# Kernel tuning notes

Measured on AMD Instinct MI355X. Metric: run time of the kernel, lower is better.

Reference implementation:

```python
import jax, jax.numpy as jnp
import numpy as np

EMB = 64
NUM_LAYERS = 2


def _mlp_embed(x, shift, scale, w1, b1, w2, b2):
    # PreNormLayer: (x + shift) * scale, then Linear-ReLU-Linear-ReLU
    x = (x + shift) * scale
    x = jax.nn.relu(x @ w1 + b1)
    return jax.nn.relu(x @ w2 + b2)


def _sage_conv(x_src, x_dst, src_idx, dst_idx, ll_w, ll_b, lr_w):
    # PyG SAGEConv: mean-aggregate gathered source features at destinations,
    # out = lin_l(mean) + lin_r(x_dst); lin_l has bias, lin_r does not.
    n_dst = x_dst.shape[0]
    msgs = x_src[src_idx]                                   # [E, D] gather
    ssum = jax.ops.segment_sum(msgs, dst_idx, num_segments=n_dst)
    cnt = jax.ops.segment_sum(jnp.ones(src_idx.shape[0], x_src.dtype),
                              dst_idx, num_segments=n_dst)
    mean = ssum / jnp.maximum(cnt, 1.0)[:, None]            # [n_dst, D]
    return mean @ ll_w + ll_b + x_dst @ lr_w


def setup_inputs() -> dict:
    key = jax.random.key(0)
    ks = jax.random.split(key, 20)
    n_cons, n_var, n_edges = 100_000, 200_000, 2_000_000
    cons_nf, var_nf, edge_nf = 5, 19, 1

    def lin(k, fan_in, fan_out):
        return jax.random.normal(k, (fan_in, fan_out), jnp.float32) / np.sqrt(fan_in)

    inp = {
        'cons_x': jax.random.normal(ks[0], (n_cons, cons_nf), jnp.float32),
        'var_x': jax.random.normal(ks[1], (n_var, var_nf), jnp.float32),
        'edge_attr': jax.random.normal(ks[2], (n_edges, edge_nf), jnp.float32),
        'edge_index': jnp.stack([
            jax.random.randint(ks[3], (n_edges,), 0, n_cons),
            jax.random.randint(ks[4], (n_edges,), 0, n_var)]).astype(jnp.int64),
        # constraint embedding MLP
        'cons_shift': 0.1 * jax.random.normal(ks[5], (cons_nf,), jnp.float32),
        'cons_scale': 1.0 + 0.1 * jax.random.normal(ks[6], (cons_nf,), jnp.float32),
        'cons_w1': lin(ks[7], cons_nf, EMB),
        'cons_b1': jnp.zeros((EMB,), jnp.float32),
        'cons_w2': lin(ks[8], EMB, EMB),
        'cons_b2': jnp.zeros((EMB,), jnp.float32),
        # variable embedding MLP
        'var_shift': 0.1 * jax.random.normal(ks[9], (var_nf,), jnp.float32),
        'var_scale': 1.0 + 0.1 * jax.random.normal(ks[10], (var_nf,), jnp.float32),
        'var_w1': lin(ks[11], var_nf, EMB),
        'var_b1': jnp.zeros((EMB,), jnp.float32),
        'var_w2': lin(ks[12], EMB, EMB),
        'var_b2': jnp.zeros((EMB,), jnp.float32),
        # edge PreNorm (computed but unused for conv_type='sage', as in source)
        'edge_shift': 0.1 * jax.random.normal(ks[13], (edge_nf,), jnp.float32),
        'edge_scale': 1.0 + 0.1 * jax.random.normal(ks[14], (edge_nf,), jnp.float32),
        # SAGEConv weights: [layer, direction(0: cons->var, 1: var->cons), in, out]
        'conv_ll_w': jax.random.normal(ks[15], (NUM_LAYERS, 2, EMB, EMB), jnp.float32) / np.sqrt(EMB),
        'conv_ll_b': jnp.zeros((NUM_LAYERS, 2, EMB), jnp.float32),
        'conv_lr_w': jax.random.normal(ks[16], (NUM_LAYERS, 2, EMB, EMB), jnp.float32) / np.sqrt(EMB),
    }
    return inp


def reference(cons_x, var_x, edge_attr, edge_index,
              cons_shift, cons_scale, cons_w1, cons_b1, cons_w2, cons_b2,
              var_shift, var_scale, var_w1, var_b1, var_w2, var_b2,
              edge_shift, edge_scale, conv_ll_w, conv_ll_b, conv_lr_w):
    x_c = _mlp_embed(cons_x, cons_shift, cons_scale, cons_w1, cons_b1, cons_w2, cons_b2)
    x_v = _mlp_embed(var_x, var_shift, var_scale, var_w1, var_b1, var_w2, var_b2)
    edge_feat = (edge_attr + edge_shift) * edge_scale  # unused for SAGE (faithful to source)
    del edge_feat
    src, dst = edge_index[0], edge_index[1]  # constraint -> variable
    for l in range(NUM_LAYERS):
        new_v = _sage_conv(x_c, x_v, src, dst, conv_ll_w[l, 0], conv_ll_b[l, 0], conv_lr_w[l, 0])
        new_c = _sage_conv(x_v, x_c, dst, src, conv_ll_w[l, 1], conv_ll_b[l, 1], conv_lr_w[l, 1])
        x_c, x_v = jax.nn.relu(new_c), jax.nn.relu(new_v)
    return x_v
```

## Files before the change

kernel.cpp:

```cpp
#include <hip/hip_runtime.h>

#define EMB 64
#define CH 4096


static __device__ __forceinline__ unsigned short f2bf(float x) {
    union { float f; unsigned u; } v; v.f = x;
    unsigned r = v.u + 0x7fffu + ((v.u >> 16) & 1u);
    return (unsigned short)(r >> 16);
}
static __device__ __forceinline__ float bflo(unsigned w) {
    union { unsigned u; float f; } v; v.u = w << 16; return v.f;
}
static __device__ __forceinline__ float bfhi(unsigned w) {
    union { unsigned u; float f; } v; v.u = w & 0xffff0000u; return v.f;
}

__global__ __launch_bounds__(256) void zero_int_kernel(int* __restrict__ p, int n) {
    int i = blockIdx.x * 256 + threadIdx.x;
    if (i < n) p[i] = 0;
}

__global__ __launch_bounds__(256) void scan_buckets_kernel(
    int* __restrict__ bc, int nbc, int* __restrict__ bv, int nbv, int E)
{
    __shared__ int sc[256];
    int t = threadIdx.x;
    {
        int v0 = (2 * t < nbc) ? bc[2 * t] : 0;
        int v1 = (2 * t + 1 < nbc) ? bc[2 * t + 1] : 0;
        sc[t] = v0 + v1;
        __syncthreads();
        for (int off = 1; off < 256; off <<= 1) {
            int x = (t >= off) ? sc[t - off] : 0;
            __syncthreads();
            sc[t] += x;
            __syncthreads();
        }
        int ex = (t > 0) ? sc[t - 1] : 0;
        if (2 * t < nbc) bc[2 * t] = ex;
        if (2 * t + 1 < nbc) bc[2 * t + 1] = ex + v0;
        if (t == 0) bc[nbc] = E;
        __syncthreads();
    }
    {
        int v0 = (2 * t < nbv) ? bv[2 * t] : 0;
        int v1 = (2 * t + 1 < nbv) ? bv[2 * t + 1] : 0;
        sc[t] = v0 + v1;
        __syncthreads();
        for (int off = 1; off < 256; off <<= 1) {
            int x = (t >= off) ? sc[t - off] : 0;
            __syncthreads();
            sc[t] += x;
            __syncthreads();
        }
        int ex = (t > 0) ? sc[t - 1] : 0;
        if (2 * t < nbv) bv[2 * t] = ex;
        if (2 * t + 1 < nbv) bv[2 * t + 1] = ex + v0;
        if (t == 0) bv[nbv] = E;
    }
}

__global__ __launch_bounds__(256) void bin_edges_kernel(
    const int* __restrict__ src, const int* __restrict__ dst, int E,
    int* __restrict__ gcur_c, int* __restrict__ gcur_v,
    unsigned* __restrict__ tmp_c, unsigned* __restrict__ tmp_v,
    int shc, int shv, int NBC, int NBV, int SLOTC, int SLOTV)
{
    __shared__ int hc[512], hv[512];
    int t = threadIdx.x;
    int base = blockIdx.x * CH;
    int n = min(CH, E - base);
    unsigned mc = (1u << shc) - 1u, mv = (1u << shv) - 1u;

    for (int i = t; i < NBC; i += 256) hc[i] = 0;
    for (int i = t; i < NBV; i += 256) hv[i] = 0;
    __syncthreads();

    int ss[16], dd[16];
#pragma unroll
    for (int q = 0; q < 16; ++q) {
        int li = t + q * 256;
        bool ok = li < n;
        ss[q] = ok ? src[base + li] : -1;
        dd[q] = ok ? dst[base + li] : -1;
        if (ok) {
            atomicAdd(&hc[ss[q] >> shc], 1);
            atomicAdd(&hv[dd[q] >> shv], 1);
        }
    }
    __syncthreads();

    for (int i = t; i < NBC; i += 256) {
        int c = hc[i];
        hc[i] = c ? (i * SLOTC + atomicAdd(&gcur_c[i], c)) : 0;
    }
    for (int i = t; i < NBV; i += 256) {
        int c = hv[i];
        hv[i] = c ? (i * SLOTV + atomicAdd(&gcur_v[i], c)) : 0;
    }
    __syncthreads();

#pragma unroll
    for (int q = 0; q < 16; ++q) {
        int li = t + q * 256;
        if (li < n) {
            unsigned s = (unsigned)ss[q], d = (unsigned)dd[q];
            int pc = atomicAdd(&hc[s >> shc], 1);
            tmp_c[pc] = ((s & mc) << 23) | d;
            int pv = atomicAdd(&hv[d >> shv], 1);
            tmp_v[pv] = ((d & mv) << 23) | s;
        }
    }
}

__global__ __launch_bounds__(256) void regroup2_dual_kernel(
    const unsigned* __restrict__ tmpA, const int* __restrict__ bbA,
    int* __restrict__ rpA, int* __restrict__ adjA, int nAn, int shA, int nbA, int slotA,
    const unsigned* __restrict__ tmpB, const int* __restrict__ bbB,
    int* __restrict__ rpB, int* __restrict__ adjB, int nBn, int shB, int nbB, int slotB, int E)
{
    __shared__ int cnt[512];
    __shared__ int offs[512];
    __shared__ int sc[256];
    const unsigned* tmp; const int* bb; int* rp; int* adj; int n_nodes, sh, nb, b, slot;
    if ((int)blockIdx.x < nbA) {
        tmp = tmpA; bb = bbA; rp = rpA; adj = adjA; n_nodes = nAn; sh = shA; nb = nbA; slot = slotA; b = blockIdx.x;
    } else {
        tmp = tmpB; bb = bbB; rp = rpB; adj = adjB; n_nodes = nBn; sh = shB; nb = nbB; slot = slotB; b = blockIdx.x - nbA;
    }
    int t = threadIdx.x;
    int node0 = b << sh;
    int node1 = min(node0 + (1 << sh), n_nodes);
    int nn = node1 - node0;
    for (int i = t; i < nn; i += 256) cnt[i] = 0;
    __syncthreads();
    int adjbase = bb[b];
    int cntb = bb[b + 1] - adjbase;
    int sbeg = b * slot;
    for (int e = sbeg + t; e < sbeg + cntb; e += 256)
        atomicAdd(&cnt[tmp[e] >> 23], 1);
    __syncthreads();
    int v0 = (2 * t < nn) ? cnt[2 * t] : 0;
    int v1 = (2 * t + 1 < nn) ? cnt[2 * t + 1] : 0;
    sc[t] = v0 + v1;
    __syncthreads();
    for (int off = 1; off < 256; off <<= 1) {
        int x = (t >= off) ? sc[t - off] : 0;
        __syncthreads();
        sc[t] += x;
        __syncthreads();
    }
    int ex = (t > 0) ? sc[t - 1] : 0;
    if (2 * t < nn) offs[2 * t] = ex;
    if (2 * t + 1 < nn) offs[2 * t + 1] = ex + v0;
    __syncthreads();
    for (int i = t; i < nn; i += 256) {
        rp[node0 + i] = adjbase + offs[i];
        cnt[i] = 0;
    }
    if (b == nb - 1 && t == 0) rp[n_nodes] = E;
    __syncthreads();
    for (int e = sbeg + t; e < sbeg + cntb; e += 256) {
        unsigned p = tmp[e];
        int d = (int)(p >> 23);
        int r = atomicAdd(&cnt[d], 1);
        adj[adjbase + offs[d] + r] = (int)(p & 0x7fffffu);
    }
}

template <int NF>
__device__ __forceinline__ void embed_body(
    float* hs, float* un,
    const float* __restrict__ x, const float* __restrict__ shift, const float* __restrict__ scale,
    const float* __restrict__ w1, const float* __restrict__ b1,
    const float* __restrict__ w2, const float* __restrict__ b2,
    const float* __restrict__ wll, const float* __restrict__ wlr,
    unsigned short* __restrict__ tb, float* __restrict__ u, int n, int bid)
{
    int t = threadIdx.x;
    long row0 = (long)bid * 64;
    int nrow = (n - row0 < 64) ? (int)(n - row0) : 64;

    float* xs  = un;
    float* w1s = un + NF * 68;

    for (int i = t; i < NF * EMB; i += 256) w1s[i] = w1[i];
    for (int i = t; i < 64 * NF; i += 256) {
        int r = i / NF, k = i - r * NF;
        float v = (r < nrow) ? x[row0 * NF + i] : 0.f;
        xs[k * 68 + r] = (v + shift[k]) * scale[k];
    }
    int r0 = (t >> 4) * 4;
    int c0 = (t & 15) * 4;
    float4 b1v = *(const float4*)&b1[c0];
    float4 b2v = *(const float4*)&b2[c0];
    __syncthreads();

    float a[4][4];
#pragma unroll
    for (int i = 0; i < 4; ++i)
#pragma unroll
        for (int j = 0; j < 4; ++j) a[i][j] = 0.f;
#pragma unroll
    for (int k = 0; k < NF; ++k) {
        float4 xv = *(const float4*)&xs[k * 68 + r0];
        float4 wv = *(const float4*)&w1s[k * EMB + c0];
        float xa[4] = {xv.x, xv.y, xv.z, xv.w};
        float wa[4] = {wv.x, wv.y, wv.z, wv.w};
#pragma unroll
        for (int i = 0; i < 4; ++i)
#pragma unroll
            for (int j = 0; j < 4; ++j)
                a[i][j] = fmaf(xa[i], wa[j], a[i][j]);
    }
    __syncthreads();
    {
        float ba[4] = {b1v.x, b1v.y, b1v.z, b1v.w};
#pragma unroll
        for (int j = 0; j < 4; ++j) {
            float4 o;
            o.x = fmaxf(a[0][j] + ba[j], 0.f);
            o.y = fmaxf(a[1][j] + ba[j], 0.f);
            o.z = fmaxf(a[2][j] + ba[j], 0.f);
            o.w = fmaxf(a[3][j] + ba[j], 0.f);
            *(float4*)&hs[(c0 + j) * 68 + r0] = o;
        }
    }
    {
        const float4* wg = (const float4*)w2;
        float4* wl = (float4*)un;
#pragma unroll
        for (int q = 0; q < 4; ++q) wl[t + q * 256] = wg[t + q * 256];
    }
    __syncthreads();

#pragma unroll
    for (int i = 0; i < 4; ++i)
#pragma unroll
        for (int j = 0; j < 4; ++j) a[i][j] = 0.f;
#pragma unroll 8
    for (int k = 0; k < EMB; ++k) {
        float4 xv = *(const float4*)&hs[k * 68 + r0];
        float4 wv = *(const float4*)&un[k * EMB + c0];
        float xa[4] = {xv.x, xv.y, xv.z, xv.w};
        float wa[4] = {wv.x, wv.y, wv.z, wv.w};
#pragma unroll
        for (int i = 0; i < 4; ++i)
#pragma unroll
            for (int j = 0; j < 4; ++j)
                a[i][j] = fmaf(xa[i], wa[j], a[i][j]);
    }
    __syncthreads();
    {
        float ba[4] = {b2v.x, b2v.y, b2v.z, b2v.w};
#pragma unroll
        for (int j = 0; j < 4; ++j) {
            float4 o;
            o.x = fmaxf(a[0][j] + ba[j], 0.f);
            o.y = fmaxf(a[1][j] + ba[j], 0.f);
            o.z = fmaxf(a[2][j] + ba[j], 0.f);
            o.w = fmaxf(a[3][j] + ba[j], 0.f);
            *(float4*)&hs[(c0 + j) * 68 + r0] = o;
        }
    }
    {
        const float4* wg = (const float4*)wll;
        float4* wl = (float4*)un;
#pragma unroll
        for (int q = 0; q < 4; ++q) wl[t + q * 256] = wg[t + q * 256];
    }
    __syncthreads();

#pragma unroll
    for (int i = 0; i < 4; ++i)
#pragma unroll
        for (int j = 0; j < 4; ++j) a[i][j] = 0.f;
#pragma unroll 8
    for (int k = 0; k < EMB; ++k) {
        float4 xv = *(const float4*)&hs[k * 68 + r0];
        float4 wv = *(const float4*)&un[k * EMB + c0];
        float xa[4] = {xv.x, xv.y, xv.z, xv.w};
        float wa[4] = {wv.x, wv.y, wv.z, wv.w};
#pragma unroll
        for (int i = 0; i < 4; ++i)
#pragma unroll
            for (int j = 0; j < 4; ++j)
                a[i][j] = fmaf(xa[i], wa[j], a[i][j]);
    }
    __syncthreads();
    {
        const float4* wg = (const float4*)wlr;
        float4* wl = (float4*)un;
#pragma unroll
        for (int q = 0; q < 4; ++q) wl[t + q * 256] = wg[t + q * 256];
    }
#pragma unroll
    for (int i = 0; i < 4; ++i) {
        long gr = row0 + r0 + i;
        if (gr < n) {
            ushort4 o;
            o.x = f2bf(a[i][0]); o.y = f2bf(a[i][1]);
            o.z = f2bf(a[i][2]); o.w = f2bf(a[i][3]);
            *(ushort4*)(tb + gr * EMB + c0) = o;
        }
    }
    __syncthreads();

#pragma unroll
    for (int i = 0; i < 4; ++i)
#pragma unroll
        for (int j = 0; j < 4; ++j) a[i][j] = 0.f;
#pragma unroll 8
    for (int k = 0; k < EMB; ++k) {
        float4 xv = *(const float4*)&hs[k * 68 + r0];
        float4 wv = *(const float4*)&un[k * EMB + c0];
        float xa[4] = {xv.x, xv.y, xv.z, xv.w};
        float wa[4] = {wv.x, wv.y, wv.z, wv.w};
#pragma unroll
        for (int i = 0; i < 4; ++i)
#pragma unroll
            for (int j = 0; j < 4; ++j)
                a[i][j] = fmaf(xa[i], wa[j], a[i][j]);
    }
#pragma unroll
    for (int i = 0; i < 4; ++i) {
        long gr = row0 + r0 + i;
        if (gr < n)
            *(float4*)&u[gr * EMB + c0] = make_float4(a[i][0], a[i][1], a[i][2], a[i][3]);
    }
}

template <int NFA, int NFB>
__global__ __launch_bounds__(256) void embed_dual_kernel(
    const float* xA, const float* shA, const float* scA,
    const float* w1A, const float* b1A, const float* w2A, const float* b2A,
    const float* wllA, const float* wlrA, unsigned short* tbA, float* uA, int nA,
    const float* xB, const float* shB, const float* scB,
    const float* w1B, const float* b1B, const float* w2B, const float* b2B,
    const float* wllB, const float* wlrB, unsigned short* tbB, float* uB, int nB,
    int split)
{
    __shared__ __align__(16) float hs[EMB * 68];
    __shared__ __align__(16) float un[4096];
    if ((int)blockIdx.x < split)
        embed_body<NFA>(hs, un, xA, shA, scA, w1A, b1A, w2A, b2A, wllA, wlrA, tbA, uA, nA, blockIdx.x);
    else
        embed_body<NFB>(hs, un, xB, shB, scB, w1B, b1B, w2B, b2B, wllB, wlrB, tbB, uB, nB, blockIdx.x - split);
}

__global__ __launch_bounds__(256) void gemm64_dual_kernel(
    const float* __restrict__ XA, int nA, const float* __restrict__ WA, unsigned short* __restrict__ CA,
    const float* __restrict__ XB, int nB, const float* __restrict__ WB, float* __restrict__ CB, int split)
{
    __shared__ __align__(16) float xs[EMB * 68];
    __shared__ __align__(16) float w1s[EMB * EMB];

    const float* X; const float* W; int n; int bid; bool bf;
    if ((int)blockIdx.x < split) { X = XA; W = WA; n = nA; bid = blockIdx.x; bf = true; }
    else { X = XB; W = WB; n = nB; bid = blockIdx.x - split; bf = false; }

    int t = threadIdx.x;
    {
        int r = t >> 2;
        int cs = (t & 3) * 16;
        long gr = (long)bid * 64 + r;
        float4 v[4];
        if (gr < n) {
            const float4* sp = (const float4*)(X + gr * EMB + cs);
#pragma unroll
            for (int q = 0; q < 4; ++q) v[q] = sp[q];
        } else {
            float4 z = make_float4(0.f, 0.f, 0.f, 0.f);
#pragma unroll
            for (int q = 0; q < 4; ++q) v[q] = z;
        }
#pragma unroll
        for (int q = 0; q < 4; ++q) {
            xs[(cs + q * 4 + 0) * 68 + r] = v[q].x;
            xs[(cs + q * 4 + 1) * 68 + r] = v[q].y;
            xs[(cs + q * 4 + 2) * 68 + r] = v[q].z;
            xs[(cs + q * 4 + 3) * 68 + r] = v[q].w;
        }
        const float4* wg = (const float4*)W;
        float4* wl = (float4*)w1s;
#pragma unroll
        for (int q = 0; q < 4; ++q) wl[t + q * 256] = wg[t + q * 256];
    }
    __syncthreads();

    int r0 = (t >> 4) * 4;
    int c0 = (t & 15) * 4;
    float acc[4][4] = {{0.f}};
#pragma unroll 8
    for (int k = 0; k < EMB; ++k) {
        float4 xv = *(const float4*)&xs[k * 68 + r0];
        float4 wv = *(const float4*)&w1s[k * EMB + c0];
        float xa[4] = {xv.x, xv.y, xv.z, xv.w};
        float wa[4] = {wv.x, wv.y, wv.z, wv.w};
#pragma unroll
        for (int i = 0; i < 4; ++i)
#pragma unroll
            for (int j = 0; j < 4; ++j)
                acc[i][j] = fmaf(xa[i], wa[j], acc[i][j]);
    }

#pragma unroll
    for (int i = 0; i < 4; ++i) {
        long gr = (long)bid * 64 + r0 + i;
        if (gr < n) {
            if (bf) {
                ushort4 o;
                o.x = f2bf(acc[i][0]); o.y = f2bf(acc[i][1]);
                o.z = f2bf(acc[i][2]); o.w = f2bf(acc[i][3]);
                *(ushort4*)(CA + gr * EMB + c0) = o;
            } else {
                *(float4*)(CB + gr * EMB + c0) =
                    make_float4(acc[i][0], acc[i][1], acc[i][2], acc[i][3]);
            }
        }
    }
}

__global__ __launch_bounds__(256) void agg_rmw_kernel(
    const unsigned short* __restrict__ tbl, const int* __restrict__ rowptr,
    const int* __restrict__ adj, const float* __restrict__ bias,
    float* __restrict__ out, int n_dst)
{
    int lane = threadIdx.x & 63;
    int node = blockIdx.x * 4 + (threadIdx.x >> 6);
    if (node >= n_dst) return;
    int p = lane & 7;
    int g = lane >> 3;
    int beg = rowptr[node];
    int end = rowptr[node + 1];
    const uint4* tb = (const uint4*)tbl;
    float a0 = 0.f, a1 = 0.f, a2 = 0.f, a3 = 0.f;
    float a4 = 0.f, a5 = 0.f, a6 = 0.f, a7 = 0.f;
    int e = beg + g;
    for (; e + 8 < end; e += 16) {
        int r0 = adj[e];
        int r1 = adj[e + 8];
        uint4 w0 = tb[(long)r0 * 8 + p];
        uint4 w1 = tb[(long)r1 * 8 + p];
        a0 += bflo(w0.x) + bflo(w1.x);
        a1 += bfhi(w0.x) + bfhi(w1.x);
        a2 += bflo(w0.y) + bflo(w1.y);
        a3 += bfhi(w0.y) + bfhi(w1.y);
        a4 += bflo(w0.z) + bflo(w1.z);
        a5 += bfhi(w0.z) + bfhi(w1.z);
        a6 += bflo(w0.w) + bflo(w1.w);
        a7 += bfhi(w0.w) + bfhi(w1.w);
    }
    if (e < end) {
        uint4 w0 = tb[(long)adj[e] * 8 + p];
        a0 += bflo(w0.x); a1 += bfhi(w0.x);
        a2 += bflo(w0.y); a3 += bfhi(w0.y);
        a4 += bflo(w0.z); a5 += bfhi(w0.z);
        a6 += bflo(w0.w); a7 += bfhi(w0.w);
    }
    a0 += __shfl_xor(a0, 8); a0 += __shfl_xor(a0, 16); a0 += __shfl_xor(a0, 32);
    a1 += __shfl_xor(a1, 8); a1 += __shfl_xor(a1, 16); a1 += __shfl_xor(a1, 32);
    a2 += __shfl_xor(a2, 8); a2 += __shfl_xor(a2, 16); a2 += __shfl_xor(a2, 32);
    a3 += __shfl_xor(a3, 8); a3 += __shfl_xor(a3, 16); a3 += __shfl_xor(a3, 32);
    a4 += __shfl_xor(a4, 8); a4 += __shfl_xor(a4, 16); a4 += __shfl_xor(a4, 32);
    a5 += __shfl_xor(a5, 8); a5 += __shfl_xor(a5, 16); a5 += __shfl_xor(a5, 32);
    a6 += __shfl_xor(a6, 8); a6 += __shfl_xor(a6, 16); a6 += __shfl_xor(a6, 32);
    a7 += __shfl_xor(a7, 8); a7 += __shfl_xor(a7, 16); a7 += __shfl_xor(a7, 32);
    if (g == 0) {
        int cnt = end - beg;
        float inv = 1.f / (float)(cnt > 0 ? cnt : 1);
        const float4* bp = (const float4*)bias + 2 * p;
        float4 bv0 = bp[0], bv1 = bp[1];
        float4* op = (float4*)(out + (long)node * EMB) + 2 * p;
        float4 ov0 = op[0], ov1 = op[1];
        float4 o0, o1;
        o0.x = fmaxf(a0 * inv + bv0.x + ov0.x, 0.f);
        o0.y = fmaxf(a1 * inv + bv0.y + ov0.y, 0.f);
        o0.z = fmaxf(a2 * inv + bv0.z + ov0.z, 0.f);
        o0.w = fmaxf(a3 * inv + bv0.w + ov0.w, 0.f);
        o1.x = fmaxf(a4 * inv + bv1.x + ov1.x, 0.f);
        o1.y = fmaxf(a5 * inv + bv1.y + ov1.y, 0.f);
        o1.z = fmaxf(a6 * inv + bv1.z + ov1.z, 0.f);
        o1.w = fmaxf(a7 * inv + bv1.w + ov1.w, 0.f);
        op[0] = o0;
        op[1] = o1;
    }
}

extern "C" void kernel_launch(void* const* d_in, const int* in_sizes, int n_in,
                              void* d_out, int out_size, void* d_ws, size_t ws_size,
                              hipStream_t stream) {
    const float* cons_x     = (const float*)d_in[0];
    const float* var_x      = (const float*)d_in[1];
    const int*   eidx       = (const int*)d_in[3];
    const float* cons_shift = (const float*)d_in[4];
    const float* cons_scale = (const float*)d_in[5];
    const float* cons_w1    = (const float*)d_in[6];
    const float* cons_b1    = (const float*)d_in[7];
    const float* cons_w2    = (const float*)d_in[8];
    const float* cons_b2    = (const float*)d_in[9];
    const float* var_shift  = (const float*)d_in[10];
    const float* var_scale  = (const float*)d_in[11];
    const float* var_w1     = (const float*)d_in[12];
    const float* var_b1     = (const float*)d_in[13];
    const float* var_w2     = (const float*)d_in[14];
    const float* var_b2     = (const float*)d_in[15];
    const float* ll_w       = (const float*)d_in[18];
    const float* ll_b       = (const float*)d_in[19];
    const float* lr_w       = (const float*)d_in[20];

    const int nC = in_sizes[0] / 5;
    const int nV = in_sizes[1] / 19;
    const int E  = in_sizes[3] / 2;
    const int* src = eidx;
    const int* dst = eidx + E;

    int shc = 0; while ((nC >> shc) >= 512) ++shc;
    int shv = 0; while ((nV >> shv) >= 512) ++shv;
    const int NBC = (nC + (1 << shc) - 1) >> shc;
    const int NBV = (nV + (1 << shv) - 1) >> shv;

    char* w = (char*)d_ws;
    auto alloc = [&](size_t bytes) {
        char* p = w;
        w += (bytes + 255) & ~(size_t)255;
        return p;
    };
    float* x_c = (float*)alloc((size_t)nC * EMB * 4);
    float* x_v = (float*)alloc((size_t)nV * EMB * 4);
    float* t_c = (float*)alloc((size_t)nC * EMB * 4);
    float* t_v = (float*)alloc((size_t)nV * EMB * 4);
    unsigned* tmp_c = (unsigned*)t_c;
    unsigned* tmp_v = (unsigned*)t_v;
    unsigned short* tb_c = (unsigned short*)t_c;
    unsigned short* tb_v = (unsigned short*)t_v;
    int* rp_v  = (int*)alloc((size_t)(nV + 1) * 4);
    int* rp_c  = (int*)alloc((size_t)(nC + 1) * 4);
    int* adj_v = (int*)alloc((size_t)E * 4);
    int* adj_c = (int*)alloc((size_t)E * 4);
    int* bkt   = (int*)alloc(2048 * 4);
    int* gcur_c = bkt;
    int* gcur_v = bkt + 1024;

    auto slot_for = [&](int NB, size_t cap_ints) {
        long s = 2L * E / NB;
        s = (s + 255) & ~255L;
        if (s < 4096) s = 4096;
        long cap = (long)(cap_ints / NB) & ~255L;
        if (s > cap) s = cap;
        return (int)s;
    };
    const int SLOTC = slot_for(NBC, (size_t)nC * EMB);
    const int SLOTV = slot_for(NBV, (size_t)nV * EMB);

    auto llw = [&](int l, int d) { return ll_w + (size_t)(l * 2 + d) * EMB * EMB; };
    auto lrw = [&](int l, int d) { return lr_w + (size_t)(l * 2 + d) * EMB * EMB; };
    auto llb = [&](int l, int d) { return ll_b + (size_t)(l * 2 + d) * EMB; };

    zero_int_kernel<<<8, 256, 0, stream>>>(bkt, 2048);
    bin_edges_kernel<<<(E + CH - 1) / CH, 256, 0, stream>>>(src, dst, E, gcur_c, gcur_v,
                                                            tmp_c, tmp_v, shc, shv, NBC, NBV,
                                                            SLOTC, SLOTV);
    scan_buckets_kernel<<<1, 256, 0, stream>>>(gcur_c, NBC, gcur_v, NBV, E);
    regroup2_dual_kernel<<<NBV + NBC, 256, 0, stream>>>(
        tmp_v, gcur_v, rp_v, adj_v, nV, shv, NBV, SLOTV,
        tmp_c, gcur_c, rp_c, adj_c, nC, shc, NBC, SLOTC, E);

    int gc = (nC + 63) / 64, gv = (nV + 63) / 64;
    embed_dual_kernel<5, 19><<<gc + gv, 256, 0, stream>>>(
        cons_x, cons_shift, cons_scale, cons_w1, cons_b1, cons_w2, cons_b2,
        llw(0, 0), lrw(0, 1), tb_c, x_c, nC,
        var_x, var_shift, var_scale, var_w1, var_b1, var_w2, var_b2,
        llw(0, 1), lrw(0, 0), tb_v, x_v, nV,
        gc);

    int gv4 = (nV + 3) / 4, gc4 = (nC + 3) / 4;
    agg_rmw_kernel<<<gv4, 256, 0, stream>>>(tb_c, rp_v, adj_v, llb(0, 0), x_v, nV);
    agg_rmw_kernel<<<gc4, 256, 0, stream>>>(tb_v, rp_c, adj_c, llb(0, 1), x_c, nC);

    gemm64_dual_kernel<<<gc + gv, 256, 0, stream>>>(
        x_c, nC, llw(1, 0), tb_c,
        x_v, nV, lrw(1, 0), (float*)d_out, gc);

    agg_rmw_kernel<<<gv4, 256, 0, stream>>>(tb_c, rp_v, adj_v, llb(1, 0), (float*)d_out, nV);
}
```

Before: 439.3 us.

## Use 16 threads per node in aggregation and XOR-swizzle embed shared tile

The aggregation kernel now assigns 16 lanes per destination node instead of a full 64-lane wavefront. With average degrees of about 10 or 20, most lanes in the old mapping sat idle, and the new mapping also cuts the shuffle reduction to one step. Separately, the embed kernel's hidden-activation shared tile moves from a padded stride-68 layout to an XOR-swizzled float4 layout to reduce LDS bank conflicts. The trade-off is less memory-level parallelism per node, since each group now has only two outstanding gathers per iteration.

Result: faster. 388.4 us (-11.6%).

```diff
diff --git a/kernel.cpp b/kernel.cpp
--- a/kernel.cpp
+++ b/kernel.cpp
@@ -171,7 +171,7 @@
 
 template <int NF>
 __device__ __forceinline__ void embed_body(
-    float* hs, float* un,
+    float4* hsf, float* un,
     const float* __restrict__ x, const float* __restrict__ shift, const float* __restrict__ scale,
     const float* __restrict__ w1, const float* __restrict__ b1,
     const float* __restrict__ w2, const float* __restrict__ b2,
@@ -191,7 +191,8 @@
         float v = (r < nrow) ? x[row0 * NF + i] : 0.f;
         xs[k * 68 + r] = (v + shift[k]) * scale[k];
     }
-    int r0 = (t >> 4) * 4;
+    int rb = t >> 4;
+    int r0 = rb * 4;
     int c0 = (t & 15) * 4;
     float4 b1v = *(const float4*)&b1[c0];
     float4 b2v = *(const float4*)&b2[c0];
@@ -219,12 +220,13 @@
         float ba[4] = {b1v.x, b1v.y, b1v.z, b1v.w};
 #pragma unroll
         for (int j = 0; j < 4; ++j) {
+            int c = c0 + j;
             float4 o;
             o.x = fmaxf(a[0][j] + ba[j], 0.f);
             o.y = fmaxf(a[1][j] + ba[j], 0.f);
             o.z = fmaxf(a[2][j] + ba[j], 0.f);
             o.w = fmaxf(a[3][j] + ba[j], 0.f);
-            *(float4*)&hs[(c0 + j) * 68 + r0] = o;
+            hsf[c * 16 + (rb ^ (c & 15))] = o;
         }
     }
     {
@@ -241,7 +243,7 @@
         for (int j = 0; j < 4; ++j) a[i][j] = 0.f;
 #pragma unroll 8
     for (int k = 0; k < EMB; ++k) {
-        float4 xv = *(const float4*)&hs[k * 68 + r0];
+        float4 xv = hsf[k * 16 + (rb ^ (k & 15))];
         float4 wv = *(const float4*)&un[k * EMB + c0];
         float xa[4] = {xv.x, xv.y, xv.z, xv.w};
         float wa[4] = {wv.x, wv.y, wv.z, wv.w};
@@ -256,12 +258,13 @@
         float ba[4] = {b2v.x, b2v.y, b2v.z, b2v.w};
 #pragma unroll
         for (int j = 0; j < 4; ++j) {
+            int c = c0 + j;
             float4 o;
             o.x = fmaxf(a[0][j] + ba[j], 0.f);
             o.y = fmaxf(a[1][j] + ba[j], 0.f);
             o.z = fmaxf(a[2][j] + ba[j], 0.f);
             o.w = fmaxf(a[3][j] + ba[j], 0.f);
-            *(float4*)&hs[(c0 + j) * 68 + r0] = o;
+            hsf[c * 16 + (rb ^ (c & 15))] = o;
         }
     }
     {
@@ -278,7 +281,7 @@
         for (int j = 0; j < 4; ++j) a[i][j] = 0.f;
 #pragma unroll 8
     for (int k = 0; k < EMB; ++k) {
-        float4 xv = *(const float4*)&hs[k * 68 + r0];
+        float4 xv = hsf[k * 16 + (rb ^ (k & 15))];
         float4 wv = *(const float4*)&un[k * EMB + c0];
         float xa[4] = {xv.x, xv.y, xv.z, xv.w};
         float wa[4] = {wv.x, wv.y, wv.z, wv.w};
@@ -313,7 +316,7 @@
         for (int j = 0; j < 4; ++j) a[i][j] = 0.f;
 #pragma unroll 8
     for (int k = 0; k < EMB; ++k) {
-        float4 xv = *(const float4*)&hs[k * 68 + r0];
+        float4 xv = hsf[k * 16 + (rb ^ (k & 15))];
         float4 wv = *(const float4*)&un[k * EMB + c0];
         float xa[4] = {xv.x, xv.y, xv.z, xv.w};
         float wa[4] = {wv.x, wv.y, wv.z, wv.w};
@@ -341,12 +344,12 @@
     const float* wllB, const float* wlrB, unsigned short* tbB, float* uB, int nB,
     int split)
 {
-    __shared__ __align__(16) float hs[EMB * 68];
+    __shared__ float4 hsf[1024];
     __shared__ __align__(16) float un[4096];
     if ((int)blockIdx.x < split)
-        embed_body<NFA>(hs, un, xA, shA, scA, w1A, b1A, w2A, b2A, wllA, wlrA, tbA, uA, nA, blockIdx.x);
+        embed_body<NFA>(hsf, un, xA, shA, scA, w1A, b1A, w2A, b2A, wllA, wlrA, tbA, uA, nA, blockIdx.x);
     else
-        embed_body<NFB>(hs, un, xB, shB, scB, w1B, b1B, w2B, b2B, wllB, wlrB, tbB, uB, nB, blockIdx.x - split);
+        embed_body<NFB>(hsf, un, xB, shB, scB, w1B, b1B, w2B, b2B, wllB, wlrB, tbB, uB, nB, blockIdx.x - split);
 }
 
 __global__ __launch_bounds__(256) void gemm64_dual_kernel(
@@ -427,20 +430,21 @@
     const int* __restrict__ adj, const float* __restrict__ bias,
     float* __restrict__ out, int n_dst)
 {
-    int lane = threadIdx.x & 63;
-    int node = blockIdx.x * 4 + (threadIdx.x >> 6);
+    int t = threadIdx.x;
+    int node = blockIdx.x * 16 + (t >> 4);
     if (node >= n_dst) return;
-    int p = lane & 7;
-    int g = lane >> 3;
+    int sub = t & 15;
+    int p = sub & 7;
+    int g = sub >> 3;
     int beg = rowptr[node];
     int end = rowptr[node + 1];
     const uint4* tb = (const uint4*)tbl;
     float a0 = 0.f, a1 = 0.f, a2 = 0.f, a3 = 0.f;
     float a4 = 0.f, a5 = 0.f, a6 = 0.f, a7 = 0.f;
     int e = beg + g;
-    for (; e + 8 < end; e += 16) {
+    for (; e + 2 < end; e += 4) {
         int r0 = adj[e];
-        int r1 = adj[e + 8];
+        int r1 = adj[e + 2];
         uint4 w0 = tb[(long)r0 * 8 + p];
         uint4 w1 = tb[(long)r1 * 8 + p];
         a0 += bflo(w0.x) + bflo(w1.x);
@@ -459,14 +463,14 @@
         a4 += bflo(w0.z); a5 += bfhi(w0.z);
         a6 += bflo(w0.w); a7 += bfhi(w0.w);
     }
-    a0 += __shfl_xor(a0, 8); a0 += __shfl_xor(a0, 16); a0 += __shfl_xor(a0, 32);
-    a1 += __shfl_xor(a1, 8); a1 += __shfl_xor(a1, 16); a1 += __shfl_xor(a1, 32);
-    a2 += __shfl_xor(a2, 8); a2 += __shfl_xor(a2, 16); a2 += __shfl_xor(a2, 32);
-    a3 += __shfl_xor(a3, 8); a3 += __shfl_xor(a3, 16); a3 += __shfl_xor(a3, 32);
-    a4 += __shfl_xor(a4, 8); a4 += __shfl_xor(a4, 16); a4 += __shfl_xor(a4, 32);
-    a5 += __shfl_xor(a5, 8); a5 += __shfl_xor(a5, 16); a5 += __shfl_xor(a5, 32);
-    a6 += __shfl_xor(a6, 8); a6 += __shfl_xor(a6, 16); a6 += __shfl_xor(a6, 32);
-    a7 += __shfl_xor(a7, 8); a7 += __shfl_xor(a7, 16); a7 += __shfl_xor(a7, 32);
+    a0 += __shfl_xor(a0, 8);
+    a1 += __shfl_xor(a1, 8);
+    a2 += __shfl_xor(a2, 8);
+    a3 += __shfl_xor(a3, 8);
+    a4 += __shfl_xor(a4, 8);
+    a5 += __shfl_xor(a5, 8);
+    a6 += __shfl_xor(a6, 8);
+    a7 += __shfl_xor(a7, 8);
     if (g == 0) {
         int cnt = end - beg;
         float inv = 1.f / (float)(cnt > 0 ? cnt : 1);
@@ -575,13 +579,13 @@
         llw(0, 1), lrw(0, 0), tb_v, x_v, nV,
         gc);
 
-    int gv4 = (nV + 3) / 4, gc4 = (nC + 3) / 4;
-    agg_rmw_kernel<<<gv4, 256, 0, stream>>>(tb_c, rp_v, adj_v, llb(0, 0), x_v, nV);
-    agg_rmw_kernel<<<gc4, 256, 0, stream>>>(tb_v, rp_c, adj_c, llb(0, 1), x_c, nC);
+    int gv16 = (nV + 15) / 16, gc16 = (nC + 15) / 16;
+    agg_rmw_kernel<<<gv16, 256, 0, stream>>>(tb_c, rp_v, adj_v, llb(0, 0), x_v, nV);
+    agg_rmw_kernel<<<gc16, 256, 0, stream>>>(tb_v, rp_c, adj_c, llb(0, 1), x_c, nC);
 
     gemm64_dual_kernel<<<gc + gv, 256, 0, stream>>>(
         x_c, nC, llw(1, 0), tb_c,
         x_v, nV, lrw(1, 0), (float*)d_out, gc);
 
-    agg_rmw_kernel<<<gv4, 256, 0, stream>>>(tb_c, rp_v, adj_v, llb(1, 0), (float*)d_out, nV);
-}
+    agg_rmw_kernel<<<gv16, 256, 0, stream>>>(tb_c, rp_v, adj_v, llb(1, 0), (float*)d_out, nV);
+}
```
